# Performance work log

Measured on AMD Instinct MI355X. Metric: run time of the kernel, lower is better.

## Reference

```python
import jax, jax.numpy as jnp
import numpy as np

N_NODES = 100000
N_EDGES = 1600000
IN_F = 128
OUT_F = 32
HEADS = 2
NEG_SLOPE = 0.2  # DGL GATConv default leaky_relu negative slope


def setup_inputs() -> dict:
    key = jax.random.key(0)
    ks = jax.random.split(key, 12)
    x = jax.random.normal(ks[0], (N_NODES, IN_F), dtype=jnp.float32)
    src = jax.random.randint(ks[1], (N_EDGES,), 0, N_NODES, dtype=jnp.int32)
    dst = jax.random.randint(ks[2], (N_EDGES,), 0, N_NODES, dtype=jnp.int32)
    # GATConv params: fc weight [IN_F, HEADS*OUT_F], attn_l/attn_r [HEADS, OUT_F], bias [HEADS*OUT_F]
    s = 1.0 / np.sqrt(IN_F)
    W = jax.random.normal(ks[3], (IN_F, HEADS * OUT_F), dtype=jnp.float32) * s
    attn_l = jax.random.normal(ks[4], (HEADS, OUT_F), dtype=jnp.float32) * s
    attn_r = jax.random.normal(ks[5], (HEADS, OUT_F), dtype=jnp.float32) * s
    bias_gat = jnp.zeros((HEADS * OUT_F,), dtype=jnp.float32)
    # MLPPredictor: lin1 (2*OUT_F -> OUT_F), lin2 (OUT_F -> 1)
    s1 = 1.0 / np.sqrt(2 * OUT_F)
    W1 = jax.random.normal(ks[6], (2 * OUT_F, OUT_F), dtype=jnp.float32) * s1
    b1 = jnp.zeros((OUT_F,), dtype=jnp.float32)
    s2 = 1.0 / np.sqrt(OUT_F)
    W2 = jax.random.normal(ks[7], (OUT_F, 1), dtype=jnp.float32) * s2
    b2 = jnp.zeros((1,), dtype=jnp.float32)
    return {"x": x, "W": W, "attn_l": attn_l, "attn_r": attn_r,
            "bias_gat": bias_gat, "W1": W1, "b1": b1, "W2": W2, "b2": b2,
            "src": src, "dst": dst}


def _forward(x, W, attn_l, attn_r, bias_gat, W1, b1, W2, b2, src, dst):
    # --- GATConv(in, out, 2 heads) ---
    feat = (x @ W).reshape(N_NODES, HEADS, OUT_F)           # [N,H,F]
    el = jnp.einsum('nhf,hf->nh', feat, attn_l)             # [N,H]
    er = jnp.einsum('nhf,hf->nh', feat, attn_r)             # [N,H]
    e = jax.nn.leaky_relu(el[src] + er[dst], NEG_SLOPE)     # [E,H]
    # edge softmax over incoming edges of each dst node (numerically stable)
    m = jax.ops.segment_max(e, dst, num_segments=N_NODES)   # [N,H]
    ex = jnp.exp(e - m[dst])                                # [E,H]
    denom = jax.ops.segment_sum(ex, dst, num_segments=N_NODES)  # [N,H]
    alpha = ex / denom[dst]                                 # [E,H]
    msg = feat[src] * alpha[:, :, None]                     # [E,H,F]
    rst = jax.ops.segment_sum(msg, dst, num_segments=N_NODES)   # [N,H,F]
    rst = rst + bias_gat.reshape(HEADS, OUT_F)
    h = jax.nn.relu(jnp.mean(rst, axis=1))                  # [N,F]
    # --- MLPPredictor: per-edge concat(src,dst) -> lin1 -> lin2 (no activation) ---
    hcat = jnp.concatenate([h[src], h[dst]], axis=1)        # [E,2F]
    score = (hcat @ W1 + b1) @ W2 + b2                      # [E,1]
    return score


def reference(x, W, attn_l, attn_r, bias_gat, W1, b1, W2, b2, src, dst):
    return _forward(x, W, attn_l, attn_r, bias_gat, W1, b1, W2, b2, src, dst)
```

## Files before the change

kernel.cpp:

```cpp
#include <hip/hip_runtime.h>
#include <hip/hip_fp16.h>

#define N_NODES 100000
#define N_EDGES 1600000
#define IN_F 128
#define OUT_F 32
#define HEADS 2
#define HO 64

#define NBUCK 782
#define BIN_BLOCKS 200
#define BIN_THREADS 1024
#define EPB (N_EDGES / BIN_BLOCKS)
#define CAP 36
#define LCAP 2368

__global__ void feat_k(const float* __restrict__ x, const float* __restrict__ W,
                       const float* __restrict__ attn_l, const float* __restrict__ attn_r,
                       __half* __restrict__ feat16, float* __restrict__ el, float* __restrict__ er,
                       const float* __restrict__ W1, const float* __restrict__ b1,
                       const float* __restrict__ W2, const float* __restrict__ b2,
                       float* __restrict__ wcomb, float* __restrict__ ccomb){
  __shared__ __align__(16) float Ws[IN_F*HO];
  __shared__ __align__(16) float xs[64*132];
  int tid = threadIdx.x;
  if (blockIdx.x == 0){
    if (tid < HO){
      float a = 0.f;
      for (int k = 0; k < OUT_F; ++k) a = fmaf(W1[tid*OUT_F + k], W2[k], a);
      wcomb[tid] = a;
    }
    if (tid == HO){
      float a = 0.f;
      for (int k = 0; k < OUT_F; ++k) a = fmaf(b1[k], W2[k], a);
      *ccomb = a + b2[0];
    }
  }
  int node0 = blockIdx.x*64;
  for (int i = tid; i < 2048; i += 256)
    ((float4*)Ws)[i] = ((const float4*)W)[i];
  for (int i = tid; i < 2048; i += 256){
    int ln = i >> 5, kq = i & 31;
    int n = node0 + ln;
    float4 v = (n < N_NODES) ? ((const float4*)x)[(size_t)n*32 + kq]
                             : make_float4(0.f,0.f,0.f,0.f);
    *(float4*)&xs[ln*132 + kq*4] = v;
  }
  __syncthreads();

  int nq = tid >> 4, cq = tid & 15;
  int n0 = nq*4, c0 = cq*4;
  float acc[4][4] = {{0.f,0.f,0.f,0.f},{0.f,0.f,0.f,0.f},{0.f,0.f,0.f,0.f},{0.f,0.f,0.f,0.f}};

  for (int k = 0; k < IN_F; k += 4){
    float xk[4][4];
    #pragma unroll
    for (int j = 0; j < 4; ++j){
      float4 t = *(const float4*)&xs[(n0+j)*132 + k];
      xk[j][0]=t.x; xk[j][1]=t.y; xk[j][2]=t.z; xk[j][3]=t.w;
    }
    #pragma unroll
    for (int d = 0; d < 4; ++d){
      float4 w4 = *(const float4*)&Ws[(k+d)*HO + c0];
      #pragma unroll
      for (int j = 0; j < 4; ++j){
        acc[j][0] = fmaf(xk[j][d], w4.x, acc[j][0]);
        acc[j][1] = fmaf(xk[j][d], w4.y, acc[j][1]);
        acc[j][2] = fmaf(xk[j][d], w4.z, acc[j][2]);
        acc[j][3] = fmaf(xk[j][d], w4.w, acc[j][3]);
      }
    }
  }

  float4 al4 = *(const float4*)&attn_l[c0];
  float4 ar4 = *(const float4*)&attn_r[c0];
  #pragma unroll
  for (int j = 0; j < 4; ++j){
    int n = node0 + n0 + j;
    float p = acc[j][0]*al4.x + acc[j][1]*al4.y + acc[j][2]*al4.z + acc[j][3]*al4.w;
    float q = acc[j][0]*ar4.x + acc[j][1]*ar4.y + acc[j][2]*ar4.z + acc[j][3]*ar4.w;
    #pragma unroll
    for (int off = 4; off; off >>= 1){ p += __shfl_xor(p, off); q += __shfl_xor(q, off); }
    if (n < N_NODES){
      __half2 h01 = __float22half2_rn(make_float2(acc[j][0], acc[j][1]));
      __half2 h23 = __float22half2_rn(make_float2(acc[j][2], acc[j][3]));
      union { uint2 u; __half2 h[2]; } pk; pk.h[0]=h01; pk.h[1]=h23;
      *(uint2*)&feat16[(size_t)n*HO + c0] = pk.u;
      if ((cq & 7) == 0){
        int h = cq >> 3;
        el[n*HEADS + h] = p;
        er[n*HEADS + h] = q;
      }
    }
  }
}

__global__ void bin_k(const int* __restrict__ src, const int* __restrict__ dst,
                      const float* __restrict__ el, const float* __restrict__ er,
                      int* __restrict__ counts, uint2* __restrict__ stg){
  __shared__ int cnt[NBUCK];
  int tid = threadIdx.x, blk = blockIdx.x;
  for (int i = tid; i < NBUCK; i += BIN_THREADS) cnt[i] = 0;
  __syncthreads();
  const int4* s4p = (const int4*)(src + blk*EPB);
  const int4* d4p = (const int4*)(dst + blk*EPB);
  for (int i = tid; i < EPB/4; i += BIN_THREADS){
    int4 s4 = s4p[i];
    int4 d4 = d4p[i];
    int ss[4] = {s4.x, s4.y, s4.z, s4.w};
    int dd[4] = {d4.x, d4.y, d4.z, d4.w};
    #pragma unroll
    for (int u = 0; u < 4; ++u){
      int s = ss[u], d = dd[u];
      float2 elv = *(const float2*)&el[s*HEADS];
      float2 erv = *(const float2*)&er[d*HEADS];
      float t0 = elv.x + erv.x, t1 = elv.y + erv.y;
      t0 = t0 > 0.f ? t0 : 0.2f*t0;
      t1 = t1 > 0.f ? t1 : 0.2f*t1;
      __half2 ex2 = __float22half2_rn(make_float2(__expf(t0), __expf(t1)));
      int b = d >> 7;
      int slot = atomicAdd(&cnt[b], 1);
      if (slot < CAP)
        stg[((size_t)blk*NBUCK + b)*CAP + slot] =
          make_uint2(((unsigned int)s << 7) | (unsigned int)(d & 127),
                     *(const unsigned int*)&ex2);
    }
  }
  __syncthreads();
  for (int i = tid; i < NBUCK; i += BIN_THREADS)
    counts[blk*NBUCK + i] = cnt[i] < CAP ? cnt[i] : CAP;
}

__global__ void __launch_bounds__(512, 8) scatter_agg_k(
                              const int* __restrict__ counts, const uint2* __restrict__ stg,
                              const __half* __restrict__ feat16, const float* __restrict__ bias,
                              const float* __restrict__ wcomb,
                              float* __restrict__ s1, float* __restrict__ s2){
  __shared__ uint2 lsev_raw[LCAP];
  __shared__ uint2 lsev[LCAP];
  __shared__ int hist[128];
  __shared__ int start[128];
  __shared__ int cur[128];
  __shared__ float dsum[256];
  __shared__ int wtot[2];
  __shared__ int ltotal;
  int b = blockIdx.x;
  int tid = threadIdx.x;
  int w = tid >> 6, lane = tid & 63;
  if (tid < 128) hist[tid] = 0;
  if (tid < 256) dsum[tid] = 0.f;
  if (tid == 0) ltotal = 0;
  __syncthreads();

  int grp = tid >> 3, gl = tid & 7;
  for (int blk = grp; blk < BIN_BLOCKS; blk += 64){
    int n = counts[blk*NBUCK + b];
    int base = 0;
    if (gl == 0 && n) base = atomicAdd(&ltotal, n);
    base = __shfl(base, (lane & 56));
    const uint2* seg = stg + ((size_t)blk*NBUCK + b)*CAP;
    for (int j = gl; j < n; j += 8){
      uint2 r = seg[j];
      int dl = r.x & 127;
      atomicAdd(&hist[dl], 1);
      float2 e = __half22float2(*(const __half2*)&r.y);
      atomicAdd(&dsum[dl], e.x);
      atomicAdd(&dsum[128 + dl], e.y);
      if (base + j < LCAP) lsev_raw[base + j] = r;
    }
  }
  __syncthreads();

  int v = 0, inc = 0;
  if (tid < 128){
    v = hist[tid];
    inc = v;
    #pragma unroll
    for (int off = 1; off < 64; off <<= 1){
      int t = __shfl_up(inc, off);
      if (lane >= off) inc += t;
    }
    if (lane == 63) wtot[w] = inc;
  }
  __syncthreads();
  if (tid == 0){ int t0 = wtot[0]; wtot[0] = 0; wtot[1] = t0; }
  __syncthreads();
  if (tid < 128){
    int excl = wtot[w] + inc - v;
    start[tid] = excl;
    cur[tid] = excl;
  }
  __syncthreads();

  int tot = ltotal < LCAP ? ltotal : LCAP;
  for (int i = tid; i < tot; i += 512){
    uint2 r = lsev_raw[i];
    int pos = atomicAdd(&cur[r.x & 127], 1);
    lsev[pos] = make_uint2(r.x >> 7, r.y);
  }
  __syncthreads();

  int g  = lane >> 4;
  int c4 = lane & 15;
  int h  = (c4 >= 8);
  float b0v = bias[c4*4 + 0], b1v = bias[c4*4 + 1], b2v = bias[c4*4 + 2], b3v = bias[c4*4 + 3];
  int f0 = (c4 & 7)*4;
  float w0 = wcomb[f0], w1 = wcomb[f0+1], w2 = wcomb[f0+2], w3 = wcomb[f0+3];
  float u0 = wcomb[32+f0], u1 = wcomb[32+f0+1], u2 = wcomb[32+f0+2], u3 = wcomb[32+f0+3];
  for (int i = 0; i < 16; ++i){
    int nl = w*16 + i;
    int node = (b << 7) + nl;
    if (node >= N_NODES) break;
    int s0 = start[nl];
    int deg = cur[nl] - s0;
    float sh = h ? dsum[128 + nl] : dsum[nl];
    float rh = sh > 0.f ? 1.f/sh : 0.f;

    float a0=0.f, a1=0.f, a2=0.f, a3=0.f;
    for (int j0 = 0; j0 < deg; j0 += 16){
      int jA = j0 + g, jB = j0 + 4 + g, jC = j0 + 8 + g, jD = j0 + 12 + g;
      float alA=0.f, alB=0.f, alC=0.f, alD=0.f;
      int snA=0, snB=0, snC=0, snD=0;
      if (jA < deg){ uint2 r = lsev[s0+jA]; snA = r.x;
        float2 e = __half22float2(*(const __half2*)&r.y); alA = (h?e.y:e.x)*rh; }
      if (jB < deg){ uint2 r = lsev[s0+jB]; snB = r.x;
        float2 e = __half22float2(*(const __half2*)&r.y); alB = (h?e.y:e.x)*rh; }
      if (jC < deg){ uint2 r = lsev[s0+jC]; snC = r.x;
        float2 e = __half22float2(*(const __half2*)&r.y); alC = (h?e.y:e.x)*rh; }
      if (jD < deg){ uint2 r = lsev[s0+jD]; snD = r.x;
        float2 e = __half22float2(*(const __half2*)&r.y); alD = (h?e.y:e.x)*rh; }
      uint2 vA = *(const uint2*)(feat16 + (size_t)snA*HO + c4*4);
      uint2 vB = *(const uint2*)(feat16 + (size_t)snB*HO + c4*4);
      uint2 vC = *(const uint2*)(feat16 + (size_t)snC*HO + c4*4);
      uint2 vD = *(const uint2*)(feat16 + (size_t)snD*HO + c4*4);
      float2 fA01 = __half22float2(*(const __half2*)&vA.x);
      float2 fA23 = __half22float2(*(const __half2*)&vA.y);
      float2 fB01 = __half22float2(*(const __half2*)&vB.x);
      float2 fB23 = __half22float2(*(const __half2*)&vB.y);
      float2 fC01 = __half22float2(*(const __half2*)&vC.x);
      float2 fC23 = __half22float2(*(const __half2*)&vC.y);
      float2 fD01 = __half22float2(*(const __half2*)&vD.x);
      float2 fD23 = __half22float2(*(const __half2*)&vD.y);
      a0 = fmaf(alA, fA01.x, a0); a0 = fmaf(alB, fB01.x, a0);
      a0 = fmaf(alC, fC01.x, a0); a0 = fmaf(alD, fD01.x, a0);
      a1 = fmaf(alA, fA01.y, a1); a1 = fmaf(alB, fB01.y, a1);
      a1 = fmaf(alC, fC01.y, a1); a1 = fmaf(alD, fD01.y, a1);
      a2 = fmaf(alA, fA23.x, a2); a2 = fmaf(alB, fB23.x, a2);
      a2 = fmaf(alC, fC23.x, a2); a2 = fmaf(alD, fD23.x, a2);
      a3 = fmaf(alA, fA23.y, a3); a3 = fmaf(alB, fB23.y, a3);
      a3 = fmaf(alC, fC23.y, a3); a3 = fmaf(alD, fD23.y, a3);
    }
    a0 += __shfl_xor(a0, 16); a1 += __shfl_xor(a1, 16); a2 += __shfl_xor(a2, 16); a3 += __shfl_xor(a3, 16);
    a0 += __shfl_xor(a0, 32); a1 += __shfl_xor(a1, 32); a2 += __shfl_xor(a2, 32); a3 += __shfl_xor(a3, 32);
    a0 += b0v; a1 += b1v; a2 += b2v; a3 += b3v;
    float h0 = 0.5f*(a0 + __shfl_xor(a0, 8)); h0 = fmaxf(h0, 0.f);
    float h1 = 0.5f*(a1 + __shfl_xor(a1, 8)); h1 = fmaxf(h1, 0.f);
    float h2 = 0.5f*(a2 + __shfl_xor(a2, 8)); h2 = fmaxf(h2, 0.f);
    float h3 = 0.5f*(a3 + __shfl_xor(a3, 8)); h3 = fmaxf(h3, 0.f);
    float p = h0*w0 + h1*w1 + h2*w2 + h3*w3;
    float q = h0*u0 + h1*u1 + h2*u2 + h3*u3;
    #pragma unroll
    for (int off = 4; off; off >>= 1){
      p += __shfl_xor(p, off);
      q += __shfl_xor(q, off);
    }
    if (lane == 0){ s1[node] = p; s2[node] = q; }
  }
}

__global__ void edge_score_k(const int* __restrict__ src, const int* __restrict__ dst,
                             const float* __restrict__ s1, const float* __restrict__ s2,
                             const float* __restrict__ ccomb, float* __restrict__ out){
  int i = blockIdx.x*blockDim.x + threadIdx.x;
  if (i >= N_EDGES/4) return;
  int4 s4 = ((const int4*)src)[i];
  int4 d4 = ((const int4*)dst)[i];
  float c = ccomb[0];
  float4 o;
  o.x = s1[s4.x] + s2[d4.x] + c;
  o.y = s1[s4.y] + s2[d4.y] + c;
  o.z = s1[s4.z] + s2[d4.z] + c;
  o.w = s1[s4.w] + s2[d4.w] + c;
  ((float4*)out)[i] = o;
}

extern "C" void kernel_launch(void* const* d_in, const int* in_sizes, int n_in,
                              void* d_out, int out_size, void* d_ws, size_t ws_size,
                              hipStream_t stream){
  const float* x      = (const float*)d_in[0];
  const float* W      = (const float*)d_in[1];
  const float* attn_l = (const float*)d_in[2];
  const float* attn_r = (const float*)d_in[3];
  const float* bias   = (const float*)d_in[4];
  const float* W1     = (const float*)d_in[5];
  const float* b1     = (const float*)d_in[6];
  const float* W2     = (const float*)d_in[7];
  const float* b2     = (const float*)d_in[8];
  const int*   src    = (const int*)d_in[9];
  const int*   dst    = (const int*)d_in[10];
  float* out = (float*)d_out;

  float* ws = (float*)d_ws;
  size_t off = 0;
  __half* feat16 = (__half*)(ws + off); off += (size_t)N_NODES*HO/2;
  float*  el     = ws + off; off += (size_t)N_NODES*HEADS;
  float*  er     = ws + off; off += (size_t)N_NODES*HEADS;
  float*  s1     = ws + off; off += N_NODES;
  float*  s2     = ws + off; off += N_NODES;
  float*  wcomb  = ws + off; off += 64;
  float*  ccomb  = ws + off; off += 64;
  int*    counts = (int*)(ws + off); off += (size_t)BIN_BLOCKS*NBUCK;
  off = (off + 1) & ~(size_t)1;
  uint2*  stg    = (uint2*)(ws + off); off += (size_t)2*BIN_BLOCKS*NBUCK*CAP;

  feat_k<<<(N_NODES + 63)/64, 256, 0, stream>>>(x, W, attn_l, attn_r, feat16, el, er,
                                                W1, b1, W2, b2, wcomb, ccomb);
  bin_k<<<BIN_BLOCKS, BIN_THREADS, 0, stream>>>(src, dst, el, er, counts, stg);
  scatter_agg_k<<<NBUCK, 512, 0, stream>>>(counts, stg, feat16, bias, wcomb, s1, s2);
  edge_score_k<<<(N_EDGES/4 + 255)/256, 256, 0, stream>>>(src, dst, s1, s2, ccomb, out);
}
```

Before: 260.6 us.

## Drop raw LDS staging buffer and compute softmax denominator during aggregation

Removes the lsev_raw shared buffer and the dsum atomics. The staged edges are now read from global memory twice: once (x-word only) to build the histogram and again to scatter directly into lsev. The softmax denominator is accumulated inside the gather loop and applied after the reduction, and the final projection is split across the two head halves so lanes 0 and 8 write s1 and s2 with fewer shuffles. Halving LDS use should raise occupancy and removes the float shared atomics, at the cost of a second global read of the staging data.

After: 251.1 us. 3.7% less time.

```diff
diff --git a/kernel.cpp b/kernel.cpp
--- a/kernel.cpp
+++ b/kernel.cpp
@@ -136,37 +136,24 @@
                               const __half* __restrict__ feat16, const float* __restrict__ bias,
                               const float* __restrict__ wcomb,
                               float* __restrict__ s1, float* __restrict__ s2){
-  __shared__ uint2 lsev_raw[LCAP];
   __shared__ uint2 lsev[LCAP];
   __shared__ int hist[128];
   __shared__ int start[128];
   __shared__ int cur[128];
-  __shared__ float dsum[256];
   __shared__ int wtot[2];
-  __shared__ int ltotal;
   int b = blockIdx.x;
   int tid = threadIdx.x;
   int w = tid >> 6, lane = tid & 63;
   if (tid < 128) hist[tid] = 0;
-  if (tid < 256) dsum[tid] = 0.f;
-  if (tid == 0) ltotal = 0;
   __syncthreads();
 
   int grp = tid >> 3, gl = tid & 7;
   for (int blk = grp; blk < BIN_BLOCKS; blk += 64){
     int n = counts[blk*NBUCK + b];
-    int base = 0;
-    if (gl == 0 && n) base = atomicAdd(&ltotal, n);
-    base = __shfl(base, (lane & 56));
-    const uint2* seg = stg + ((size_t)blk*NBUCK + b)*CAP;
+    const unsigned int* segx = (const unsigned int*)(stg + ((size_t)blk*NBUCK + b)*CAP);
     for (int j = gl; j < n; j += 8){
-      uint2 r = seg[j];
-      int dl = r.x & 127;
-      atomicAdd(&hist[dl], 1);
-      float2 e = __half22float2(*(const __half2*)&r.y);
-      atomicAdd(&dsum[dl], e.x);
-      atomicAdd(&dsum[128 + dl], e.y);
-      if (base + j < LCAP) lsev_raw[base + j] = r;
+      unsigned int rx = segx[2*j];
+      atomicAdd(&hist[rx & 127], 1);
     }
   }
   __syncthreads();
@@ -192,11 +179,14 @@
   }
   __syncthreads();
 
-  int tot = ltotal < LCAP ? ltotal : LCAP;
-  for (int i = tid; i < tot; i += 512){
-    uint2 r = lsev_raw[i];
-    int pos = atomicAdd(&cur[r.x & 127], 1);
-    lsev[pos] = make_uint2(r.x >> 7, r.y);
+  for (int blk = grp; blk < BIN_BLOCKS; blk += 64){
+    int n = counts[blk*NBUCK + b];
+    const uint2* seg = stg + ((size_t)blk*NBUCK + b)*CAP;
+    for (int j = gl; j < n; j += 8){
+      uint2 r = seg[j];
+      int pos = atomicAdd(&cur[r.x & 127], 1);
+      if (pos < LCAP) lsev[pos] = make_uint2(r.x >> 7, r.y);
+    }
   }
   __syncthreads();
 
@@ -205,30 +195,30 @@
   int h  = (c4 >= 8);
   float b0v = bias[c4*4 + 0], b1v = bias[c4*4 + 1], b2v = bias[c4*4 + 2], b3v = bias[c4*4 + 3];
   int f0 = (c4 & 7)*4;
-  float w0 = wcomb[f0], w1 = wcomb[f0+1], w2 = wcomb[f0+2], w3 = wcomb[f0+3];
-  float u0 = wcomb[32+f0], u1 = wcomb[32+f0+1], u2 = wcomb[32+f0+2], u3 = wcomb[32+f0+3];
+  int wo = (h ? 32 : 0) + f0;
+  float m0 = wcomb[wo], m1 = wcomb[wo+1], m2 = wcomb[wo+2], m3 = wcomb[wo+3];
   for (int i = 0; i < 16; ++i){
     int nl = w*16 + i;
     int node = (b << 7) + nl;
     if (node >= N_NODES) break;
     int s0 = start[nl];
-    int deg = cur[nl] - s0;
-    float sh = h ? dsum[128 + nl] : dsum[nl];
-    float rh = sh > 0.f ? 1.f/sh : 0.f;
-
-    float a0=0.f, a1=0.f, a2=0.f, a3=0.f;
+    int e0 = cur[nl]; if (e0 > LCAP) e0 = LCAP;
+    int deg = e0 - s0; if (deg < 0) deg = 0;
+
+    float a0=0.f, a1=0.f, a2=0.f, a3=0.f, dn=0.f;
     for (int j0 = 0; j0 < deg; j0 += 16){
       int jA = j0 + g, jB = j0 + 4 + g, jC = j0 + 8 + g, jD = j0 + 12 + g;
       float alA=0.f, alB=0.f, alC=0.f, alD=0.f;
       int snA=0, snB=0, snC=0, snD=0;
       if (jA < deg){ uint2 r = lsev[s0+jA]; snA = r.x;
-        float2 e = __half22float2(*(const __half2*)&r.y); alA = (h?e.y:e.x)*rh; }
+        float2 e = __half22float2(*(const __half2*)&r.y); alA = (h?e.y:e.x); }
       if (jB < deg){ uint2 r = lsev[s0+jB]; snB = r.x;
-        float2 e = __half22float2(*(const __half2*)&r.y); alB = (h?e.y:e.x)*rh; }
+        float2 e = __half22float2(*(const __half2*)&r.y); alB = (h?e.y:e.x); }
       if (jC < deg){ uint2 r = lsev[s0+jC]; snC = r.x;
-        float2 e = __half22float2(*(const __half2*)&r.y); alC = (h?e.y:e.x)*rh; }
+        float2 e = __half22float2(*(const __half2*)&r.y); alC = (h?e.y:e.x); }
       if (jD < deg){ uint2 r = lsev[s0+jD]; snD = r.x;
-        float2 e = __half22float2(*(const __half2*)&r.y); alD = (h?e.y:e.x)*rh; }
+        float2 e = __half22float2(*(const __half2*)&r.y); alD = (h?e.y:e.x); }
+      dn += alA + alB + alC + alD;
       uint2 vA = *(const uint2*)(feat16 + (size_t)snA*HO + c4*4);
       uint2 vB = *(const uint2*)(feat16 + (size_t)snB*HO + c4*4);
       uint2 vC = *(const uint2*)(feat16 + (size_t)snC*HO + c4*4);
@@ -250,21 +240,23 @@
       a3 = fmaf(alA, fA23.y, a3); a3 = fmaf(alB, fB23.y, a3);
       a3 = fmaf(alC, fC23.y, a3); a3 = fmaf(alD, fD23.y, a3);
     }
-    a0 += __shfl_xor(a0, 16); a1 += __shfl_xor(a1, 16); a2 += __shfl_xor(a2, 16); a3 += __shfl_xor(a3, 16);
-    a0 += __shfl_xor(a0, 32); a1 += __shfl_xor(a1, 32); a2 += __shfl_xor(a2, 32); a3 += __shfl_xor(a3, 32);
-    a0 += b0v; a1 += b1v; a2 += b2v; a3 += b3v;
+    a0 += __shfl_xor(a0, 16); a1 += __shfl_xor(a1, 16);
+    a2 += __shfl_xor(a2, 16); a3 += __shfl_xor(a3, 16);
+    dn += __shfl_xor(dn, 16);
+    a0 += __shfl_xor(a0, 32); a1 += __shfl_xor(a1, 32);
+    a2 += __shfl_xor(a2, 32); a3 += __shfl_xor(a3, 32);
+    dn += __shfl_xor(dn, 32);
+    float rh = dn > 0.f ? 1.f/dn : 0.f;
+    a0 = fmaf(a0, rh, b0v); a1 = fmaf(a1, rh, b1v);
+    a2 = fmaf(a2, rh, b2v); a3 = fmaf(a3, rh, b3v);
     float h0 = 0.5f*(a0 + __shfl_xor(a0, 8)); h0 = fmaxf(h0, 0.f);
     float h1 = 0.5f*(a1 + __shfl_xor(a1, 8)); h1 = fmaxf(h1, 0.f);
     float h2 = 0.5f*(a2 + __shfl_xor(a2, 8)); h2 = fmaxf(h2, 0.f);
     float h3 = 0.5f*(a3 + __shfl_xor(a3, 8)); h3 = fmaxf(h3, 0.f);
-    float p = h0*w0 + h1*w1 + h2*w2 + h3*w3;
-    float q = h0*u0 + h1*u1 + h2*u2 + h3*u3;
-    #pragma unroll
-    for (int off = 4; off; off >>= 1){
-      p += __shfl_xor(p, off);
-      q += __shfl_xor(q, off);
-    }
-    if (lane == 0){ s1[node] = p; s2[node] = q; }
+    float r = h0*m0 + h1*m1 + h2*m2 + h3*m3;
+    r += __shfl_xor(r, 4); r += __shfl_xor(r, 2); r += __shfl_xor(r, 1);
+    if (lane == 0)      s1[node] = r;
+    else if (lane == 8) s2[node] = r;
   }
 }
 
```
